# Kernel tuning notes

Measured on AMD Instinct MI355X. Metric: run time of the kernel, lower is better.

## Reference

```python
import jax, jax.numpy as jnp
import numpy as np

B, S, D, H = 4, 2048, 1024, 16
DH = D // H


def setup_inputs() -> dict:
    key = jax.random.key(0)
    ks = jax.random.split(key, 6)
    scale = 1.0 / np.sqrt(D)  # xavier-ish scale for weights
    return {
        "x": jax.random.normal(ks[0], (B, S, D), dtype=jnp.float32),
        "M": jax.random.normal(ks[1], (B, D, D), dtype=jnp.float32) * scale,
        "mask": jnp.zeros((1, 1, S, S), dtype=jnp.float32),
        "Wq": jax.random.normal(ks[2], (D, D), dtype=jnp.float32) * scale,
        "Wk": jax.random.normal(ks[3], (D, D), dtype=jnp.float32) * scale,
        "Wv": jax.random.normal(ks[4], (D, D), dtype=jnp.float32) * scale,
        "Wo": jax.random.normal(ks[5], (D, D), dtype=jnp.float32) * scale,
    }


def reference(x, M, mask, Wq, Wk, Wv, Wo):
    # Projections (torch Linear: y = x @ W^T, bias=False)
    Q = jnp.einsum('bsd,ed->bse', x, Wq)
    K = jnp.einsum('bsd,ed->bse', x, Wk)
    V = jnp.einsum('bsd,ed->bse', x, Wv)
    # Archetypal metric: QM = Q @ M, per-batch bilinear transform on full d_model
    QM = jnp.einsum('bsd,bde->bse', Q, M)

    def split(t):  # [B,S,D] -> [B,H,S,DH]
        return t.reshape(B, S, H, DH).transpose(0, 2, 1, 3)

    QMh, Kh, Vh = split(QM), split(K), split(V)
    scores = jnp.einsum('bhsd,bhtd->bhst', QMh, Kh) / np.sqrt(DH)
    scores = jnp.clip(scores, -50.0, 50.0)
    scores = scores + mask  # broadcast additive mask
    attn = jax.nn.softmax(scores, axis=-1)  # dropout is identity (eval)
    out = jnp.einsum('bhst,bhtd->bhsd', attn, Vh)
    out = out.transpose(0, 2, 1, 3).reshape(B, S, D)  # merge heads
    return jnp.einsum('bsd,ed->bse', out, Wo)
```

## Files before the change

kernel.cpp:

```cpp
#include <hip/hip_runtime.h>
#include <cstdint>

typedef __attribute__((ext_vector_type(8))) short short8;
typedef __attribute__((ext_vector_type(8))) __bf16 bf16x8;
typedef __attribute__((ext_vector_type(4))) float f32x4;

__device__ __forceinline__ uint32_t cvt_pk_bf16(float lo, float hi) {
  uint32_t r;
  asm("v_cvt_pk_bf16_f32 %0, %1, %2" : "=v"(r) : "v"(lo), "v"(hi));
  return r;
}

__device__ __forceinline__ short f2bf(float f) {
  return (short)cvt_pk_bf16(f, f);
}

__device__ __forceinline__ float exp2_fast(float x) {
  return __builtin_amdgcn_exp2f(x);
}

__device__ __forceinline__ void mem_fence_compiler() {
  asm volatile("" ::: "memory");
}

__device__ __forceinline__ void gload_lds16(const void* g, void* l) {
  __builtin_amdgcn_global_load_lds(
      (const __attribute__((address_space(1))) void*)(uintptr_t)g,
      (__attribute__((address_space(3))) void*)(uint32_t)(uintptr_t)l,
      16, 0, 0);
}


__global__ __launch_bounds__(256) void cvt_f32_bf16(const float* __restrict__ s,
                                                    short* __restrict__ d, long n) {
  long i = ((long)blockIdx.x * 256 + threadIdx.x) * 8;
  if (i + 8 > n) return;
  const float4 a = *(const float4*)(s + i);
  const float4 b = *(const float4*)(s + i + 4);
  uint4 o;
  o.x = cvt_pk_bf16(a.x, a.y);
  o.y = cvt_pk_bf16(a.z, a.w);
  o.z = cvt_pk_bf16(b.x, b.y);
  o.w = cvt_pk_bf16(b.z, b.w);
  *(uint4*)(d + i) = o;
}

__global__ __launch_bounds__(256) void cvtT_M(const float* __restrict__ Msrc,
                                              short* __restrict__ Mt) {
  __shared__ short t[64][65];
  const int tid = threadIdx.x;
  const long bofs = (long)blockIdx.z * 1024 * 1024;
  const int d0 = blockIdx.x * 64, e0 = blockIdx.y * 64;
#pragma unroll
  for (int k = 0; k < 16; ++k) {
    int idx = k * 256 + tid; int r = idx >> 6, c = idx & 63;
    t[r][c] = f2bf(Msrc[bofs + (long)(d0 + r) * 1024 + e0 + c]);
  }
  __syncthreads();
#pragma unroll
  for (int k = 0; k < 16; ++k) {
    int idx = k * 256 + tid; int r = idx >> 6, c = idx & 63;
    Mt[bofs + (long)(e0 + r) * 1024 + d0 + c] = t[c][r];
  }
}

__global__ __launch_bounds__(256) void transposeV(const short* __restrict__ V,
                                                  short* __restrict__ Vt) {
  __shared__ short t[64][65];
  const int tid = threadIdx.x;
  const int s0 = blockIdx.x * 64, h = blockIdx.y;
  const long b = blockIdx.z;
  const short* src = V + (b * 2048) * 1024 + h * 64;
  short* dst = Vt + ((b * 16 + h) * 64) * 2048;
#pragma unroll
  for (int k = 0; k < 16; ++k) {
    int idx = k * 256 + tid; int r = idx >> 6, c = idx & 63;
    t[r][c] = src[(long)(s0 + r) * 1024 + c];
  }
  __syncthreads();
#pragma unroll
  for (int k = 0; k < 16; ++k) {
    int idx = k * 256 + tid; int r = idx >> 6, c = idx & 63;
    dst[(long)r * 2048 + s0 + c] = t[c][r];
  }
}

__global__ __launch_bounds__(256) void mask_flags(const float* __restrict__ mask,
                                                  int* __restrict__ flags) {
  __shared__ int f;
  const int tid = threadIdx.x;
  if (tid == 0) f = 0;
  __syncthreads();
  const int qt = blockIdx.x, tt = blockIdx.y;
  const float* base = mask + (long)qt * 64 * 2048 + tt * 64;
  const int r = tid >> 2, c = (tid & 3) * 16;
  bool nz = false;
#pragma unroll
  for (int k = 0; k < 4; ++k) {
    float4 v = *(const float4*)(base + (long)r * 2048 + c + k * 4);
    nz = nz | (v.x != 0.f) | (v.y != 0.f) | (v.z != 0.f) | (v.w != 0.f);
  }
  if (nz) f = 1;
  __syncthreads();
  if (tid == 0) flags[qt * 32 + tt] = f;
}


template <typename CT>
__global__ __launch_bounds__(256) void gemm_bt(
    const short* __restrict__ A, const short* __restrict__ B, CT* __restrict__ C,
    int M, int N, int K, long sA, long sB, long sC, float scale) {
  __shared__ __align__(16) short As[128 * 64];
  __shared__ __align__(16) short Bs[128 * 64];
  const int tid = threadIdx.x;
  const int w = tid >> 6, lane = tid & 63;
  const int wr = w >> 1, wc = w & 1;
  const int g = lane >> 4;
  const short* Ab = A + (long)blockIdx.z * sA + (long)blockIdx.x * 128 * K;
  const short* Bb = B + (long)blockIdx.z * sB + (long)blockIdx.y * 128 * K;

  f32x4 acc[4][4];
#pragma unroll
  for (int i = 0; i < 4; ++i)
#pragma unroll
    for (int j = 0; j < 4; ++j) acc[i][j] = {0.f, 0.f, 0.f, 0.f};

  const int srow8 = lane >> 3;
  const int scol8 = ((lane & 7) ^ (srow8 & 7)) * 8;

  for (int k0 = 0; k0 < K; k0 += 64) {
    __syncthreads();
#pragma unroll
    for (int c = 0; c < 4; ++c) {
      const int chunk = c * 4 + w;
      const long row = chunk * 8 + srow8;
      gload_lds16(Ab + row * K + k0 + scol8, &As[chunk * 512]);
      gload_lds16(Bb + row * K + k0 + scol8, &Bs[chunk * 512]);
    }
    __syncthreads();
#pragma unroll
    for (int s = 0; s < 2; ++s) {
      bf16x8 af[4], bfr[4];
#pragma unroll
      for (int mf = 0; mf < 4; ++mf) {
        const int r = wr * 64 + mf * 16 + (lane & 15);
        const int cb = (s * 4 + g) ^ (r & 7);
        af[mf] = *(const bf16x8*)&As[r * 64 + cb * 8];
      }
#pragma unroll
      for (int nf = 0; nf < 4; ++nf) {
        const int r = wc * 64 + nf * 16 + (lane & 15);
        const int cb = (s * 4 + g) ^ (r & 7);
        bfr[nf] = *(const bf16x8*)&Bs[r * 64 + cb * 8];
      }
#pragma unroll
      for (int mf = 0; mf < 4; ++mf)
#pragma unroll
        for (int nf = 0; nf < 4; ++nf)
          acc[mf][nf] =
              __builtin_amdgcn_mfma_f32_16x16x32_bf16(af[mf], bfr[nf], acc[mf][nf], 0, 0, 0);
    }
  }

  CT* Cb = C + (long)blockIdx.z * sC;
  const int r0 = g * 4, cc = lane & 15;
#pragma unroll
  for (int mf = 0; mf < 4; ++mf)
#pragma unroll
    for (int i = 0; i < 4; ++i) {
      const long row = (long)blockIdx.x * 128 + wr * 64 + mf * 16 + r0 + i;
#pragma unroll
      for (int nf = 0; nf < 4; ++nf) {
        const long col = (long)blockIdx.y * 128 + wc * 64 + nf * 16 + cc;
        float v = acc[mf][nf][i] * scale;
        if constexpr (__is_same(CT, short))
          Cb[row * (long)N + col] = f2bf(v);
        else
          Cb[row * (long)N + col] = v;
      }
    }
}


__global__ __launch_bounds__(512) void flash_attn(
    const short* __restrict__ QM, const short* __restrict__ Kb,
    const short* __restrict__ Vt, const float* __restrict__ mask,
    const int* __restrict__ mflags, short* __restrict__ AO) {
  constexpr int S = 2048, D = 1024, NT = S / 64;
  constexpr float LOG2E = 1.44269504088896f;
  constexpr float CLIP = 50.0f * LOG2E;
  __shared__ __align__(16) short Ks[2][64 * 64];
  __shared__ __align__(16) short Vs[2][64 * 64];
  __shared__ __align__(16) short Ps[8][16 * 64];
  const int tid = threadIdx.x;
  const int w = tid >> 6, lane = tid & 63;
  const int q = lane & 15, g = lane >> 4;
  const int q0 = blockIdx.x * 128;
  const int h = blockIdx.y;
  const long b = blockIdx.z;

  const short* QMb = QM + (b * S) * D + h * 64;
  const short* Kbp = Kb + (b * S) * D + h * 64;
  const short* Vtp = Vt + ((b * 16 + h) * 64) * S;
  const int* flagrow = mflags + ((q0 + w * 16) >> 6) * 32;

  bf16x8 qf[2];
#pragma unroll
  for (int ks = 0; ks < 2; ++ks)
    qf[ks] = *(const bf16x8*)(QMb + (long)(q0 + w * 16 + q) * D + ks * 32 + g * 8);

  bf16x8 onesf;
#pragma unroll
  for (int j = 0; j < 8; ++j) onesf[j] = (__bf16)1.0f;

  f32x4 acc[4];
#pragma unroll
  for (int f = 0; f < 4; ++f) acc[f] = {0.f, 0.f, 0.f, 0.f};
  f32x4 acc_l = {0.f, 0.f, 0.f, 0.f};

  const int srow8 = lane >> 3;
  const int scol8 = ((lane & 7) ^ (srow8 & 7)) * 8;
  short* Pw = &Ps[w][0];
  const int psw = (q & 7) << 3;

  auto STAGE = [&](int bufi, int t0) {
    const int row = w * 8 + srow8;
    gload_lds16(Kbp + (long)(t0 + row) * D + scol8, &Ks[bufi][w * 512]);
    gload_lds16(Vtp + (long)row * S + t0 + scol8, &Vs[bufi][w * 512]);
  };

  auto COMPUTE = [&](int bufi, int t0) {
    f32x4 sacc[4];
#pragma unroll
    for (int nf = 0; nf < 4; ++nf) sacc[nf] = {0.f, 0.f, 0.f, 0.f};
    __builtin_amdgcn_s_setprio(1);
#pragma unroll
    for (int ks = 0; ks < 2; ++ks) {
#pragma unroll
      for (int nf = 0; nf < 4; ++nf) {
        const int r = nf * 16 + q;
        const int blk = (ks * 4 + g) ^ (r & 7);
        bf16x8 kf = *(const bf16x8*)&Ks[bufi][r * 64 + blk * 8];
        sacc[nf] = __builtin_amdgcn_mfma_f32_16x16x32_bf16(kf, qf[ks], sacc[nf], 0, 0, 0);
      }
    }
    __builtin_amdgcn_s_setprio(0);

    float pv[4][4];
    if (__builtin_expect(flagrow[t0 >> 6], 0)) {
      const float* mrow = mask + (long)(q0 + w * 16 + q) * S + t0;
#pragma unroll
      for (int nf = 0; nf < 4; ++nf) {
        float4 mv = *(const float4*)(mrow + nf * 16 + 4 * g);
        const float* mp = &mv.x;
#pragma unroll
        for (int i = 0; i < 4; ++i)
          pv[nf][i] = exp2_fast(
              __builtin_amdgcn_fmed3f(sacc[nf][i], -CLIP, CLIP) + LOG2E * mp[i]);
      }
    } else {
#pragma unroll
      for (int nf = 0; nf < 4; ++nf)
#pragma unroll
        for (int i = 0; i < 4; ++i)
          pv[nf][i] = exp2_fast(__builtin_amdgcn_fmed3f(sacc[nf][i], -CLIP, CLIP));
    }
#pragma unroll
    for (int nf = 0; nf < 4; ++nf) {
      uint2 u;
      u.x = cvt_pk_bf16(pv[nf][0], pv[nf][1]);
      u.y = cvt_pk_bf16(pv[nf][2], pv[nf][3]);
      *(uint2*)&Pw[q * 64 + ((nf * 16 + 4 * g) ^ psw)] = u;
    }

    mem_fence_compiler();

    __builtin_amdgcn_s_setprio(1);
#pragma unroll
    for (int ts = 0; ts < 2; ++ts) {
      bf16x8 pfr = *(const bf16x8*)&Pw[q * 64 + ((ts * 32 + 8 * g) ^ psw)];
#pragma unroll
      for (int f = 0; f < 4; ++f) {
        const int vr = f * 16 + q;
        const int vblk = (ts * 4 + g) ^ (vr & 7);
        bf16x8 vf = *(const bf16x8*)&Vs[bufi][vr * 64 + vblk * 8];
        acc[f] = __builtin_amdgcn_mfma_f32_16x16x32_bf16(vf, pfr, acc[f], 0, 0, 0);
      }
      acc_l = __builtin_amdgcn_mfma_f32_16x16x32_bf16(onesf, pfr, acc_l, 0, 0, 0);
    }
    __builtin_amdgcn_s_setprio(0);
    mem_fence_compiler();
  };

  STAGE(0, 0);
  for (int it = 0; it < NT; ++it) {
    const int cur = it & 1;
    if (it + 1 < NT) {
      STAGE(cur ^ 1, (it + 1) * 64);
      asm volatile("s_waitcnt vmcnt(2)" ::: "memory");
    } else {
      asm volatile("s_waitcnt vmcnt(0)" ::: "memory");
    }
    __builtin_amdgcn_s_barrier();
    __builtin_amdgcn_sched_barrier(0);
    COMPUTE(cur, it * 64);
    __builtin_amdgcn_sched_barrier(0);
    __builtin_amdgcn_s_barrier();
  }

  const float inv = 1.0f / acc_l[0];
#pragma unroll
  for (int f = 0; f < 4; ++f) {
    uint2 u;
    u.x = cvt_pk_bf16(acc[f][0] * inv, acc[f][1] * inv);
    u.y = cvt_pk_bf16(acc[f][2] * inv, acc[f][3] * inv);
    *(uint2*)&Pw[q * 64 + ((f * 16 + 4 * g) ^ psw)] = u;
  }
  mem_fence_compiler();
  const int qr = lane >> 2, c0 = (lane & 3) * 16;
  short* AOp = AO + (b * S) * D + h * 64;
#pragma unroll
  for (int r2 = 0; r2 < 2; ++r2) {
    const int cc2 = c0 + r2 * 8;
    bf16x8 ov = *(const bf16x8*)&Pw[qr * 64 + (cc2 ^ ((qr & 7) << 3))];
    *(bf16x8*)(AOp + (long)(q0 + w * 16 + qr) * D + cc2) = ov;
  }
}


extern "C" void kernel_launch(void* const* d_in, const int* in_sizes, int n_in,
                              void* d_out, int out_size, void* d_ws, size_t ws_size,
                              hipStream_t stream) {
  const float* x = (const float*)d_in[0];
  const float* M = (const float*)d_in[1];
  const float* mask = (const float*)d_in[2];
  const float* Wq = (const float*)d_in[3];
  const float* Wk = (const float*)d_in[4];
  const float* Wv = (const float*)d_in[5];
  const float* Wo = (const float*)d_in[6];
  float* out = (float*)d_out;

  constexpr long S = 2048, D = 1024;
  constexpr long NX = 4 * S * D;
  constexpr long NW = D * D;
  constexpr float C1 = 0.125f * 1.44269504088896f;

  short* p = (short*)d_ws;
  short* xb = p;   p += NX;
  short* wkb = p;  p += NW;
  short* wvb = p;  p += NW;
  short* wob = p;  p += NW;
  short* wqt = p;  p += NW;
  short* Mtb = p;  p += 4 * NW;
  short* Gtb = p;  p += 4 * NW;
  short* Kb = p;   p += NX;
  short* Vb = p;   p += NX;
  short* QMb = p;  p += NX;
  short* Vtb = p;  p += NX;
  int* flags = (int*)p;  p += 2048;
  short* AOb = Mtb;

  cvt_f32_bf16<<<NX / 2048, 256, 0, stream>>>(x, xb, NX);
  cvt_f32_bf16<<<NW / 2048, 256, 0, stream>>>(Wk, wkb, NW);
  cvt_f32_bf16<<<NW / 2048, 256, 0, stream>>>(Wv, wvb, NW);
  cvt_f32_bf16<<<NW / 2048, 256, 0, stream>>>(Wo, wob, NW);
  cvtT_M<<<dim3(16, 16, 1), 256, 0, stream>>>(Wq, wqt);
  cvtT_M<<<dim3(16, 16, 4), 256, 0, stream>>>(M, Mtb);
  mask_flags<<<dim3(32, 32), 256, 0, stream>>>(mask, flags);

  gemm_bt<short><<<dim3(64, 8, 2), 256, 0, stream>>>(xb, wkb, Kb, 8192, 1024, 1024,
                                                     0, NW, NX, 1.0f);
  gemm_bt<short><<<dim3(8, 8, 4), 256, 0, stream>>>(Mtb, wqt, Gtb, 1024, 1024, 1024,
                                                    NW, 0, NW, 1.0f);
  gemm_bt<short><<<dim3(16, 8, 4), 256, 0, stream>>>(xb, Gtb, QMb, 2048, 1024, 1024,
                                                     S * D, NW, S * D, C1);
  transposeV<<<dim3(32, 16, 4), 256, 0, stream>>>(Vb, Vtb);
  flash_attn<<<dim3(16, 16, 4), 512, 0, stream>>>(QMb, Kb, Vtb, mask, flags, AOb);
  gemm_bt<float><<<dim3(64, 8, 1), 256, 0, stream>>>(AOb, wob, out, 8192, 1024, 1024,
                                                     0, 0, 0, 1.0f);
}
```

Measured before the change: 259.9 us.

## Load K fragments directly from global into registers and remap attention grid

K tiles are no longer staged through LDS; each wave loads its K MFMA operands straight from global memory into registers each iteration, with the vmcnt waits adjusted to match. The grid becomes 1D with a block-index remap that spreads the 8 head/batch groups across neighbouring blocks, presumably for L2/XCD locality. This halves LDS use and removes the LDS reads for K. In exchange, every wave issues redundant global loads for the same K tile, and those loads are exposed latency right before the QK MFMAs.

```diff
diff --git a/kernel.cpp b/kernel.cpp
--- a/kernel.cpp
+++ b/kernel.cpp
@@ -189,15 +189,18 @@
   constexpr int S = 2048, D = 1024, NT = S / 64;
   constexpr float LOG2E = 1.44269504088896f;
   constexpr float CLIP = 50.0f * LOG2E;
-  __shared__ __align__(16) short Ks[2][64 * 64];
   __shared__ __align__(16) short Vs[2][64 * 64];
   __shared__ __align__(16) short Ps[8][16 * 64];
   const int tid = threadIdx.x;
   const int w = tid >> 6, lane = tid & 63;
   const int q = lane & 15, g = lane >> 4;
-  const int q0 = blockIdx.x * 128;
-  const int h = blockIdx.y;
-  const long b = blockIdx.z;
+  const int p = blockIdx.x;
+  const int kx = p & 7, j = p >> 3;
+  const int m = j & 15, ghi = j >> 4;
+  const int grp = ghi * 8 + kx;
+  const int h = grp & 15;
+  const long b = grp >> 4;
+  const int q0 = m * 128;
 
   const short* QMb = QM + (b * S) * D + h * 64;
   const short* Kbp = Kb + (b * S) * D + h * 64;
@@ -211,7 +214,7 @@
 
   bf16x8 onesf;
 #pragma unroll
-  for (int j = 0; j < 8; ++j) onesf[j] = (__bf16)1.0f;
+  for (int jj = 0; jj < 8; ++jj) onesf[jj] = (__bf16)1.0f;
 
   f32x4 acc[4];
 #pragma unroll
@@ -222,28 +225,34 @@
   const int scol8 = ((lane & 7) ^ (srow8 & 7)) * 8;
   short* Pw = &Ps[w][0];
   const int psw = (q & 7) << 3;
+  const short* Kq = Kbp + (long)q * D + g * 8;
 
   auto STAGE = [&](int bufi, int t0) {
     const int row = w * 8 + srow8;
-    gload_lds16(Kbp + (long)(t0 + row) * D + scol8, &Ks[bufi][w * 512]);
     gload_lds16(Vtp + (long)row * S + t0 + scol8, &Vs[bufi][w * 512]);
   };
 
+  bf16x8 kf[2][4];
+  auto LOADK = [&](int t0) {
+    const short* Kt = Kq + (long)t0 * D;
+#pragma unroll
+    for (int nf = 0; nf < 4; ++nf)
+#pragma unroll
+      for (int ks = 0; ks < 2; ++ks)
+        kf[ks][nf] = *(const bf16x8*)(Kt + nf * 16 * D + ks * 32);
+  };
+
   auto COMPUTE = [&](int bufi, int t0) {
     f32x4 sacc[4];
 #pragma unroll
     for (int nf = 0; nf < 4; ++nf) sacc[nf] = {0.f, 0.f, 0.f, 0.f};
     __builtin_amdgcn_s_setprio(1);
 #pragma unroll
-    for (int ks = 0; ks < 2; ++ks) {
-#pragma unroll
-      for (int nf = 0; nf < 4; ++nf) {
-        const int r = nf * 16 + q;
-        const int blk = (ks * 4 + g) ^ (r & 7);
-        bf16x8 kf = *(const bf16x8*)&Ks[bufi][r * 64 + blk * 8];
-        sacc[nf] = __builtin_amdgcn_mfma_f32_16x16x32_bf16(kf, qf[ks], sacc[nf], 0, 0, 0);
-      }
-    }
+    for (int ks = 0; ks < 2; ++ks)
+#pragma unroll
+      for (int nf = 0; nf < 4; ++nf)
+        sacc[nf] =
+            __builtin_amdgcn_mfma_f32_16x16x32_bf16(kf[ks][nf], qf[ks], sacc[nf], 0, 0, 0);
     __builtin_amdgcn_s_setprio(0);
 
     float pv[4][4];
@@ -295,11 +304,12 @@
   STAGE(0, 0);
   for (int it = 0; it < NT; ++it) {
     const int cur = it & 1;
+    LOADK(it * 64);
     if (it + 1 < NT) {
       STAGE(cur ^ 1, (it + 1) * 64);
-      asm volatile("s_waitcnt vmcnt(2)" ::: "memory");
+      asm volatile("s_waitcnt vmcnt(9)" ::: "memory");
     } else {
-      asm volatile("s_waitcnt vmcnt(0)" ::: "memory");
+      asm volatile("s_waitcnt vmcnt(8)" ::: "memory");
     }
     __builtin_amdgcn_s_barrier();
     __builtin_amdgcn_sched_barrier(0);
@@ -375,7 +385,7 @@
   gemm_bt<short><<<dim3(16, 8, 4), 256, 0, stream>>>(xb, Gtb, QMb, 2048, 1024, 1024,
                                                      S * D, NW, S * D, C1);
   transposeV<<<dim3(32, 16, 4), 256, 0, stream>>>(Vb, Vtb);
-  flash_attn<<<dim3(16, 16, 4), 512, 0, stream>>>(QMb, Kb, Vtb, mask, flags, AOb);
+  flash_attn<<<dim3(1024), 512, 0, stream>>>(QMb, Kb, Vtb, mask, flags, AOb);
   gemm_bt<float><<<dim3(64, 8, 1), 256, 0, stream>>>(AOb, wob, out, 8192, 1024, 1024,
                                                      0, 0, 0, 1.0f);
 }
```

Result: slower. 426.1 us (+63.9%).
